# Kernel optimization log

Measured on AMD Instinct MI355X. Metric: run time of the kernel, lower is better.

## Reference

```python
import jax, jax.numpy as jnp
import numpy as np

B, T, C_EMBD, C_ATT = 16, 1024, 2048, 2048


def wkv(time_decay, time_first, k, v):
    """Numerically-stable RWKV WKV recurrence (matches wkv_cuda).
    time_decay/time_first: [C]; k, v: [B, T, C] -> y: [B, T, C]."""
    w = -jnp.exp(time_decay)  # [C], decay is -exp(param)
    u = time_first
    Bn, Tn, Cn = k.shape

    def step(carry, kv_t):
        aa, bb, pp = carry          # each [B, C]
        kt, vt = kv_t               # [B, C]
        ww = u + kt
        p = jnp.maximum(pp, ww)
        e1 = jnp.exp(pp - p)
        e2 = jnp.exp(ww - p)
        y = (e1 * aa + e2 * vt) / (e1 * bb + e2)
        ww2 = pp + w
        p2 = jnp.maximum(ww2, kt)
        e1b = jnp.exp(ww2 - p2)
        e2b = jnp.exp(kt - p2)
        new = (e1b * aa + e2b * vt, e1b * bb + e2b, p2)
        return new, y

    init = (jnp.zeros((Bn, Cn), k.dtype),
            jnp.zeros((Bn, Cn), k.dtype),
            jnp.full((Bn, Cn), -1e38, k.dtype))
    kT = jnp.swapaxes(k, 0, 1)  # [T, B, C]
    vT = jnp.swapaxes(v, 0, 1)
    _, ys = jax.lax.scan(step, init, (kT, vT))
    return jnp.swapaxes(ys, 0, 1)  # [B, T, C]


def setup_inputs() -> dict:
    key = jax.random.key(0)
    ks = jax.random.split(key, 10)
    xav = np.sqrt(2.0 / (C_EMBD + C_ATT))
    inp = {
        "x": jax.random.normal(ks[0], (B, T, C_EMBD), jnp.float32),
        "time_decay": jax.random.normal(ks[1], (C_ATT,), jnp.float32) * 0.02,
        "time_first": jax.random.normal(ks[2], (C_ATT,), jnp.float32) * 0.02,
        "time_mix_k": jax.random.normal(ks[3], (1, 1, C_EMBD), jnp.float32) * 0.02,
        "time_mix_v": jax.random.normal(ks[4], (1, 1, C_EMBD), jnp.float32) * 0.02,
        "time_mix_r": jax.random.normal(ks[5], (1, 1, C_EMBD), jnp.float32) * 0.02,
        "key_w": jax.random.normal(ks[6], (C_ATT, C_EMBD), jnp.float32) * xav,
        "value_w": jax.random.normal(ks[7], (C_ATT, C_EMBD), jnp.float32) * xav,
        "receptance_w": jax.random.normal(ks[8], (C_ATT, C_EMBD), jnp.float32) * xav,
        "output_w": jax.random.normal(ks[9], (C_EMBD, C_ATT), jnp.float32) * xav,
    }
    return inp


def reference(x, time_decay, time_first, time_mix_k, time_mix_v, time_mix_r,
              key_w, value_w, receptance_w, output_w):
    # time shift: xx[:, t] = x[:, t-1], xx[:, 0] = 0
    xx = jnp.pad(x, ((0, 0), (1, 0), (0, 0)))[:, :-1]
    xk = x * time_mix_k + xx * (1 - time_mix_k)
    xv = x * time_mix_v + xx * (1 - time_mix_v)
    xr = x * time_mix_r + xx * (1 - time_mix_r)
    k = jnp.einsum('btc,dc->btd', xk, key_w)
    v = jnp.einsum('btc,dc->btd', xv, value_w)
    r = jnp.einsum('btc,dc->btd', xr, receptance_w)
    sr = jax.nn.sigmoid(r)
    rwkv = sr * wkv(time_decay, time_first, k, v)
    return jnp.einsum('btd,cd->btc', rwkv, output_w)
```

## Files before the change

kernel.cpp:

```cpp
#include <hip/hip_runtime.h>
#include <hip/hip_bf16.h>

#define BB 16
#define TT 1024
#define CC 2048
#define TS 32

typedef __attribute__((ext_vector_type(4))) float f32x4;
typedef __attribute__((ext_vector_type(8))) short bf16x8;

__device__ __forceinline__ unsigned short f2bf(float f) {
  union { float f; unsigned u; } x; x.f = f;
  unsigned r = x.u + 0x7fffu + ((x.u >> 16) & 1u);
  return (unsigned short)(r >> 16);
}
__device__ __forceinline__ float bf2f(unsigned short u) {
  union { unsigned u; float f; } x; x.u = ((unsigned)u) << 16;
  return x.f;
}

__device__ __forceinline__ ushort4 mix4(float4 a, float4 b, float4 m) {
  ushort4 o;
  o.x = f2bf(a.x * m.x + b.x * (1.f - m.x));
  o.y = f2bf(a.y * m.y + b.y * (1.f - m.y));
  o.z = f2bf(a.z * m.z + b.z * (1.f - m.z));
  o.w = f2bf(a.w * m.w + b.w * (1.f - m.w));
  return o;
}

__global__ void f2bf_all(const float* __restrict__ w0, const float* __restrict__ w1,
                         const float* __restrict__ w2, const float* __restrict__ w3,
                         unsigned short* __restrict__ o0, unsigned short* __restrict__ o1,
                         unsigned short* __restrict__ o2, unsigned short* __restrict__ o3,
                         int n4each) {
  const float* ws[4] = {w0, w1, w2, w3};
  unsigned short* os[4] = {o0, o1, o2, o3};
  int total = 4 * n4each;
  for (int i = blockIdx.x * blockDim.x + threadIdx.x; i < total;
       i += gridDim.x * blockDim.x) {
    int seg = i / n4each, j = i - seg * n4each;
    float4 v = ((const float4*)ws[seg])[j];
    ushort4 o;
    o.x = f2bf(v.x); o.y = f2bf(v.y); o.z = f2bf(v.z); o.w = f2bf(v.w);
    ((ushort4*)os[seg])[j] = o;
  }
}

__global__ void mix_kernel(const float* __restrict__ x,
                           const float* __restrict__ tmk,
                           const float* __restrict__ tmv,
                           const float* __restrict__ tmr,
                           unsigned short* __restrict__ xk,
                           unsigned short* __restrict__ xv,
                           unsigned short* __restrict__ xr,
                           int t0, int Tc) {
  const int C4 = CC / 4;
  const int total = BB * Tc * C4;
  for (int g = blockIdx.x * blockDim.x + threadIdx.x; g < total;
       g += gridDim.x * blockDim.x) {
    int cg = g % C4;
    int lrow = g / C4;
    int tl = lrow % Tc;
    int b = lrow / Tc;
    int t = t0 + tl;
    size_t gidx = (size_t)(b * TT + t) * C4 + cg;
    float4 xc = ((const float4*)x)[gidx];
    float4 xp = make_float4(0.f, 0.f, 0.f, 0.f);
    if (t > 0) xp = ((const float4*)x)[gidx - C4];
    ((ushort4*)xk)[g] = mix4(xc, xp, ((const float4*)tmk)[cg]);
    ((ushort4*)xv)[g] = mix4(xc, xp, ((const float4*)tmv)[cg]);
    ((ushort4*)xr)[g] = mix4(xc, xp, ((const float4*)tmr)[cg]);
  }
}

template<bool BF16OUT>
__global__ __launch_bounds__(512, 2)
void gemm256(const unsigned short* __restrict__ A,
             const unsigned short* __restrict__ B,
             void* __restrict__ Cv, int M, int N, int K,
             int tcShift, int t0) {
  __shared__ __align__(1024) unsigned char lds[131072];
  const int tid = threadIdx.x;
  const int lane = tid & 63;
  const int wid = tid >> 6;
  const int wr = wid >> 2;
  const int wc = wid & 3;

  const int nwg = gridDim.x;
  const int cpx = nwg >> 3;
  const int bid = blockIdx.x;
  const int wg = (bid & 7) * cpx + (bid >> 3);
  const int bcolN = N >> 8;
  const int brow = wg / bcolN;
  const int bcol = wg % bcolN;

  const unsigned short* Ag = A + (size_t)(brow * 256) * K;
  const unsigned short* Bg = B + (size_t)(bcol * 256) * K;

  const int srow = tid >> 3;
  const int scolB = ((tid & 7) * 16) ^ ((srow & 7) << 4);
  const int scolE = scolB >> 1;
  const int ldsWave = wid * 1024;

#define STAGE(gbase, rowOff, ldsOff, kOff)                                     \
  __builtin_amdgcn_global_load_lds(                                            \
      (const __attribute__((address_space(1))) void*)(                         \
          (gbase) + (size_t)((rowOff) + srow) * K + (kOff) + scolE),           \
      (__attribute__((address_space(3))) void*)(lds + (ldsOff) + ldsWave),     \
      16, 0, 0)

  const int frow = lane & 15;
  const int fhi = (lane >> 4) << 4;

#define FRAG(tb, row, kk)                                                      \
  (*(const bf16x8*)(lds + (tb) + (row) * 128 +                                 \
                    ((((kk) << 6) + fhi) ^ (((row) & 7) << 4))))

  const int NT = K >> 6;

  STAGE(Bg,   0, 32768 +     0, 0);
  STAGE(Bg,  64, 32768 +  8192, 0);
  STAGE(Bg, 128, 32768 + 16384, 0);
  STAGE(Bg, 192, 32768 + 24576, 0);
  STAGE(Ag,   0,             0, 0);
  STAGE(Ag, 128,         16384, 0);
  STAGE(Ag,  64,          8192, 0);
  STAGE(Ag, 192,         24576, 0);

  f32x4 acc[8][4] = {};
  bf16x8 af[8], bfr[8];

  for (int kt = 0; kt < NT; ++kt) {
    const int p = kt & 1;
    const int Ab = p * 65536;
    const int Bb = Ab + 32768;
    const int An = (p ^ 1) * 65536;
    const int Bn = An + 32768;
    const int kN = (kt + 1) << 6;
    const bool st = (kt + 1 < NT);

    asm volatile("s_waitcnt vmcnt(2)" ::: "memory");
    __builtin_amdgcn_s_barrier();

    if (st) { STAGE(Bg, 0, Bn, kN); STAGE(Bg, 64, Bn + 8192, kN); }
#pragma unroll
    for (int m = 0; m < 4; ++m)
#pragma unroll
      for (int kk = 0; kk < 2; ++kk)
        af[m * 2 + kk] = FRAG(Ab, wr * 128 + m * 16 + frow, kk);
#pragma unroll
    for (int n = 0; n < 2; ++n)
#pragma unroll
      for (int kk = 0; kk < 2; ++kk)
        bfr[n * 2 + kk] = FRAG(Bb, wc * 64 + n * 16 + frow, kk);
    __builtin_amdgcn_s_setprio(1);
#pragma unroll
    for (int m = 0; m < 4; ++m)
#pragma unroll
      for (int n = 0; n < 2; ++n)
#pragma unroll
        for (int kk = 0; kk < 2; ++kk)
          acc[m][n] = __builtin_amdgcn_mfma_f32_16x16x32_bf16(
              af[m * 2 + kk], bfr[n * 2 + kk], acc[m][n], 0, 0, 0);
    __builtin_amdgcn_s_setprio(0);
    __builtin_amdgcn_s_barrier();

    if (st) { STAGE(Bg, 128, Bn + 16384, kN); STAGE(Bg, 192, Bn + 24576, kN); }
#pragma unroll
    for (int n = 2; n < 4; ++n)
#pragma unroll
      for (int kk = 0; kk < 2; ++kk)
        bfr[n * 2 + kk] = FRAG(Bb, wc * 64 + n * 16 + frow, kk);
    __builtin_amdgcn_s_setprio(1);
#pragma unroll
    for (int m = 0; m < 4; ++m)
#pragma unroll
      for (int n = 2; n < 4; ++n)
#pragma unroll
        for (int kk = 0; kk < 2; ++kk)
          acc[m][n] = __builtin_amdgcn_mfma_f32_16x16x32_bf16(
              af[m * 2 + kk], bfr[n * 2 + kk], acc[m][n], 0, 0, 0);
    __builtin_amdgcn_s_setprio(0);

    if (st) { asm volatile("s_waitcnt vmcnt(4)" ::: "memory"); }
    else    { asm volatile("s_waitcnt vmcnt(0)" ::: "memory"); }
    __builtin_amdgcn_s_barrier();

    if (st) { STAGE(Ag, 0, An, kN); STAGE(Ag, 128, An + 16384, kN); }
#pragma unroll
    for (int m = 0; m < 4; ++m)
#pragma unroll
      for (int kk = 0; kk < 2; ++kk)
        af[m * 2 + kk] = FRAG(Ab, wr * 128 + 64 + m * 16 + frow, kk);
    __builtin_amdgcn_s_setprio(1);
#pragma unroll
    for (int m = 0; m < 4; ++m)
#pragma unroll
      for (int n = 2; n < 4; ++n)
#pragma unroll
        for (int kk = 0; kk < 2; ++kk)
          acc[4 + m][n] = __builtin_amdgcn_mfma_f32_16x16x32_bf16(
              af[m * 2 + kk], bfr[n * 2 + kk], acc[4 + m][n], 0, 0, 0);
    __builtin_amdgcn_s_setprio(0);
    __builtin_amdgcn_s_barrier();

    if (st) { STAGE(Ag, 64, An + 8192, kN); STAGE(Ag, 192, An + 24576, kN); }
    __builtin_amdgcn_s_setprio(1);
#pragma unroll
    for (int m = 0; m < 4; ++m)
#pragma unroll
      for (int n = 0; n < 2; ++n)
#pragma unroll
        for (int kk = 0; kk < 2; ++kk)
          acc[4 + m][n] = __builtin_amdgcn_mfma_f32_16x16x32_bf16(
              af[m * 2 + kk], bfr[n * 2 + kk], acc[4 + m][n], 0, 0, 0);
    __builtin_amdgcn_s_setprio(0);
  }
#undef STAGE
#undef FRAG

  const int crow0 = (lane >> 4) << 2;
  const int ccol = lane & 15;
  const int tcMask = (1 << tcShift) - 1;
#pragma unroll
  for (int m = 0; m < 8; ++m)
#pragma unroll
    for (int n = 0; n < 4; ++n) {
      const int col = bcol * 256 + wc * 64 + n * 16 + ccol;
#pragma unroll
      for (int j = 0; j < 4; ++j) {
        int r = brow * 256 + wr * 128 + m * 16 + crow0 + j;
        int orow = ((r >> tcShift) << 10) + t0 + (r & tcMask);
        if (BF16OUT)
          ((unsigned short*)Cv)[(size_t)orow * N + col] = f2bf(acc[m][n][j]);
        else
          ((float*)Cv)[(size_t)orow * N + col] = acc[m][n][j];
      }
    }
}

__global__ void wkv_part(const float* __restrict__ time_decay,
                         const float* __restrict__ k,
                         const unsigned short* __restrict__ v,
                         float* __restrict__ paA, float* __restrict__ paB,
                         float* __restrict__ paP, int Tc) {
  int idx = blockIdx.x * blockDim.x + threadIdx.x;
  int c = idx & (CC - 1);
  int b = (idx >> 11) & (BB - 1);
  int s = idx >> 15;
  float w = -__expf(time_decay[c]);
  float aa = 0.f, bb = 0.f, pp = -1e38f;
  size_t base = ((size_t)b * Tc + s * TS) * CC + c;
  for (int t = 0; t < TS; ++t) {
    size_t off = base + (size_t)t * CC;
    float kt = k[off], vt = bf2f(v[off]);
    float ww2 = pp + w;
    float p2 = fmaxf(ww2, kt);
    float e1 = __expf(ww2 - p2), e2 = __expf(kt - p2);
    aa = e1 * aa + e2 * vt;
    bb = e1 * bb + e2;
    pp = p2;
  }
  paA[idx] = aa; paB[idx] = bb; paP[idx] = pp;
}

__global__ void wkv_comb(const float* __restrict__ time_decay,
                         const float* __restrict__ paA,
                         const float* __restrict__ paB,
                         const float* __restrict__ paP,
                         float* __restrict__ inA, float* __restrict__ inB,
                         float* __restrict__ inP,
                         float* __restrict__ state, int S, int t0) {
  int idx = blockIdx.x * blockDim.x + threadIdx.x;
  int c = idx & (CC - 1);
  float w = -__expf(time_decay[c]);
  float wTs = w * (float)TS;
  float A, Bv, P;
  if (t0 == 0) { A = 0.f; Bv = 0.f; P = -1e38f; }
  else { A = state[idx]; Bv = state[32768 + idx]; P = state[65536 + idx]; }
  for (int s = 0; s < S; ++s) {
    size_t o = (size_t)s * 32768 + idx;
    inA[o] = A; inB[o] = Bv; inP[o] = P;
    float Pd = P + wTs;
    float Ps = paP[o];
    float Pn = fmaxf(Pd, Ps);
    float e1 = __expf(Pd - Pn), e2 = __expf(Ps - Pn);
    A = e1 * A + e2 * paA[o];
    Bv = e1 * Bv + e2 * paB[o];
    P = Pn;
  }
  state[idx] = A; state[32768 + idx] = Bv; state[65536 + idx] = P;
}

__global__ void wkv_out(const float* __restrict__ time_decay,
                        const float* __restrict__ time_first,
                        const float* __restrict__ k,
                        const unsigned short* __restrict__ v,
                        const unsigned short* __restrict__ r,
                        unsigned short* __restrict__ rwkv,
                        const float* __restrict__ inA,
                        const float* __restrict__ inB,
                        const float* __restrict__ inP, int Tc) {
  int idx = blockIdx.x * blockDim.x + threadIdx.x;
  int c = idx & (CC - 1);
  int b = (idx >> 11) & (BB - 1);
  int s = idx >> 15;
  float w = -__expf(time_decay[c]);
  float u = time_first[c];
  float aa = inA[idx], bb = inB[idx], pp = inP[idx];
  size_t base = ((size_t)b * Tc + s * TS) * CC + c;
  for (int t = 0; t < TS; ++t) {
    size_t off = base + (size_t)t * CC;
    float kt = k[off], vt = bf2f(v[off]);
    float ww = u + kt;
    float p = fmaxf(pp, ww);
    float e1 = __expf(pp - p), e2 = __expf(ww - p);
    float y = (e1 * aa + e2 * vt) / (e1 * bb + e2);
    float rr = bf2f(r[off]);
    float sr = 1.f / (1.f + __expf(-rr));
    rwkv[off] = f2bf(sr * y);
    float ww2 = pp + w;
    float p2 = fmaxf(ww2, kt);
    float e1b = __expf(ww2 - p2), e2b = __expf(kt - p2);
    aa = e1b * aa + e2b * vt;
    bb = e1b * bb + e2b;
    pp = p2;
  }
}

extern "C" void kernel_launch(void* const* d_in, const int* in_sizes, int n_in,
                              void* d_out, int out_size, void* d_ws,
                              size_t ws_size, hipStream_t stream) {
  const float* x          = (const float*)d_in[0];
  const float* time_decay = (const float*)d_in[1];
  const float* time_first = (const float*)d_in[2];
  const float* tmk        = (const float*)d_in[3];
  const float* tmv        = (const float*)d_in[4];
  const float* tmr        = (const float*)d_in[5];
  const float* key_w      = (const float*)d_in[6];
  const float* value_w    = (const float*)d_in[7];
  const float* rec_w      = (const float*)d_in[8];
  const float* out_w      = (const float*)d_in[9];
  float* out = (float*)d_out;

  const size_t WW = (size_t)CC * CC;
  const size_t wtBytes = 4 * WW * 2;
  const size_t stBytes = 3 * (size_t)BB * CC * 4;

  int Tc = 1024;
  while (Tc > 32) {
    size_t chunkBytes = (size_t)BB * Tc * CC * 14;
    if (wtBytes + stBytes + chunkBytes + 1024 <= ws_size) break;
    Tc >>= 1;
  }
  const int Mc = BB * Tc;
  const size_t NC = (size_t)Mc * CC;
  const int S = Tc / TS;

  char* p = (char*)d_ws;
  unsigned short* wk  = (unsigned short*)p; p += WW * 2;
  unsigned short* wv  = (unsigned short*)p; p += WW * 2;
  unsigned short* wrr = (unsigned short*)p; p += WW * 2;
  unsigned short* wo  = (unsigned short*)p; p += WW * 2;
  float* state        = (float*)p;          p += stBytes;
  float* kbuf         = (float*)p;          p += NC * 4;
  unsigned short* vbuf= (unsigned short*)p; p += NC * 2;
  unsigned short* xk  = (unsigned short*)p; p += NC * 2;
  unsigned short* xv  = (unsigned short*)p; p += NC * 2;
  unsigned short* xr  = (unsigned short*)p; p += NC * 2;
  unsigned short* rbuf= (unsigned short*)p; p += NC * 2;
  unsigned short* rwkv = xk;

  const size_t SBt = (size_t)S * 32768;
  float* paA = (float*)xv;
  float* paB = paA + SBt;
  float* paP = paB + SBt;
  float* inA = paP + SBt;
  float* inB = inA + SBt;
  float* inP = inB + SBt;

  f2bf_all<<<2048, 256, 0, stream>>>(key_w, value_w, rec_w, out_w,
                                     wk, wv, wrr, wo, (int)(WW / 4));

  int tcShift = 0;
  while ((1 << tcShift) < Tc) ++tcShift;

  const int nwg = (Mc / 256) * (CC / 256);
  int mixBlocks = (Mc * (CC / 4) + 255) / 256;
  if (mixBlocks > 4096) mixBlocks = 4096;

  for (int t0 = 0; t0 < TT; t0 += Tc) {
    mix_kernel<<<mixBlocks, 256, 0, stream>>>(x, tmk, tmv, tmr, xk, xv, xr,
                                              t0, Tc);
    gemm256<false><<<nwg, 512, 0, stream>>>(xk, wk, kbuf, Mc, CC, CC, 10, 0);
    gemm256<true><<<nwg, 512, 0, stream>>>(xv, wv, vbuf, Mc, CC, CC, 10, 0);
    wkv_part<<<S * 128, 256, 0, stream>>>(time_decay, kbuf, vbuf,
                                          paA, paB, paP, Tc);
    gemm256<true><<<nwg, 512, 0, stream>>>(xr, wrr, rbuf, Mc, CC, CC, 10, 0);
    wkv_comb<<<128, 256, 0, stream>>>(time_decay, paA, paB, paP,
                                      inA, inB, inP, state, S, t0);
    wkv_out<<<S * 128, 256, 0, stream>>>(time_decay, time_first, kbuf, vbuf,
                                         rbuf, rwkv, inA, inB, inP, Tc);
    gemm256<false><<<nwg, 512, 0, stream>>>(rwkv, wo, out, Mc, CC, CC,
                                            tcShift, t0);
  }
}
```

Before: 740.1 us.

## Software-pipeline GEMM fragment loads across iterations and store k in bf16

Restructures the GEMM main loop so the first A/B fragments for the next k-tile are read from LDS at the end of the current iteration. The output quadrant order is reordered so fragment reads overlap MFMA work, with barriers and waitcnts moved to match. Separately, the key projection output is now written as bf16 instead of fp32, shrinking kbuf traffic and workspace size. This risks precision loss in the exponent-sensitive WKV recurrence and adds register pressure from the double fragment sets.

```diff
diff --git a/kernel.cpp b/kernel.cpp
--- a/kernel.cpp
+++ b/kernel.cpp
@@ -116,6 +116,8 @@
   (*(const bf16x8*)(lds + (tb) + (row) * 128 +                                 \
                     ((((kk) << 6) + fhi) ^ (((row) & 7) << 4))))
 
+#define FENCE asm volatile("" ::: "memory")
+
   const int NT = K >> 6;
 
   STAGE(Bg,   0, 32768 +     0, 0);
@@ -128,119 +130,134 @@
   STAGE(Ag, 192,         24576, 0);
 
   f32x4 acc[8][4] = {};
-  bf16x8 af[8], bfr[8];
+  bf16x8 af0[8], af1[8], bf0[4], bf1[4];
+
+  asm volatile("s_waitcnt vmcnt(2)" ::: "memory");
+  __builtin_amdgcn_s_barrier();
+#pragma unroll
+  for (int m = 0; m < 4; ++m)
+#pragma unroll
+    for (int kk = 0; kk < 2; ++kk)
+      af0[m * 2 + kk] = FRAG(0, wr * 128 + m * 16 + frow, kk);
+#pragma unroll
+  for (int n = 0; n < 2; ++n)
+#pragma unroll
+    for (int kk = 0; kk < 2; ++kk)
+      bf0[n * 2 + kk] = FRAG(32768, wc * 64 + n * 16 + frow, kk);
 
   for (int kt = 0; kt < NT; ++kt) {
-    const int p = kt & 1;
-    const int Ab = p * 65536;
-    const int Bb = Ab + 32768;
-    const int An = (p ^ 1) * 65536;
-    const int Bn = An + 32768;
+    const int cur = (kt & 1) << 16;
+    const int nxt = ((kt + 1) & 1) << 16;
     const int kN = (kt + 1) << 6;
     const bool st = (kt + 1 < NT);
 
-    asm volatile("s_waitcnt vmcnt(2)" ::: "memory");
-    __builtin_amdgcn_s_barrier();
-
-    if (st) { STAGE(Bg, 0, Bn, kN); STAGE(Bg, 64, Bn + 8192, kN); }
+    if (st) { STAGE(Bg, 0, nxt + 32768, kN); STAGE(Bg, 64, nxt + 32768 + 8192, kN); }
+    __builtin_amdgcn_s_setprio(1);
 #pragma unroll
     for (int m = 0; m < 4; ++m)
 #pragma unroll
+      for (int n = 0; n < 2; ++n)
+#pragma unroll
+        for (int kk = 0; kk < 2; ++kk)
+          acc[m][n] = __builtin_amdgcn_mfma_f32_16x16x32_bf16(
+              af0[m * 2 + kk], bf0[n * 2 + kk], acc[m][n], 0, 0, 0);
+    __builtin_amdgcn_s_setprio(0);
+#pragma unroll
+    for (int n = 0; n < 2; ++n)
+#pragma unroll
       for (int kk = 0; kk < 2; ++kk)
-        af[m * 2 + kk] = FRAG(Ab, wr * 128 + m * 16 + frow, kk);
-#pragma unroll
-    for (int n = 0; n < 2; ++n)
-#pragma unroll
-      for (int kk = 0; kk < 2; ++kk)
-        bfr[n * 2 + kk] = FRAG(Bb, wc * 64 + n * 16 + frow, kk);
-    __builtin_amdgcn_s_setprio(1);
-#pragma unroll
-    for (int m = 0; m < 4; ++m)
-#pragma unroll
-      for (int n = 0; n < 2; ++n)
-#pragma unroll
-        for (int kk = 0; kk < 2; ++kk)
-          acc[m][n] = __builtin_amdgcn_mfma_f32_16x16x32_bf16(
-              af[m * 2 + kk], bfr[n * 2 + kk], acc[m][n], 0, 0, 0);
-    __builtin_amdgcn_s_setprio(0);
-    __builtin_amdgcn_s_barrier();
-
-    if (st) { STAGE(Bg, 128, Bn + 16384, kN); STAGE(Bg, 192, Bn + 24576, kN); }
-#pragma unroll
-    for (int n = 2; n < 4; ++n)
-#pragma unroll
-      for (int kk = 0; kk < 2; ++kk)
-        bfr[n * 2 + kk] = FRAG(Bb, wc * 64 + n * 16 + frow, kk);
-    __builtin_amdgcn_s_setprio(1);
-#pragma unroll
-    for (int m = 0; m < 4; ++m)
-#pragma unroll
-      for (int n = 2; n < 4; ++n)
-#pragma unroll
-        for (int kk = 0; kk < 2; ++kk)
-          acc[m][n] = __builtin_amdgcn_mfma_f32_16x16x32_bf16(
-              af[m * 2 + kk], bfr[n * 2 + kk], acc[m][n], 0, 0, 0);
-    __builtin_amdgcn_s_setprio(0);
-
-    if (st) { asm volatile("s_waitcnt vmcnt(4)" ::: "memory"); }
+        bf1[n * 2 + kk] = FRAG(cur + 32768, wc * 64 + 32 + n * 16 + frow, kk);
+    FENCE;
+    if (st) { asm volatile("s_waitcnt vmcnt(2)" ::: "memory"); }
     else    { asm volatile("s_waitcnt vmcnt(0)" ::: "memory"); }
     __builtin_amdgcn_s_barrier();
 
-    if (st) { STAGE(Ag, 0, An, kN); STAGE(Ag, 128, An + 16384, kN); }
+    if (st) { STAGE(Bg, 128, nxt + 32768 + 16384, kN); STAGE(Bg, 192, nxt + 32768 + 24576, kN); }
 #pragma unroll
     for (int m = 0; m < 4; ++m)
 #pragma unroll
       for (int kk = 0; kk < 2; ++kk)
-        af[m * 2 + kk] = FRAG(Ab, wr * 128 + 64 + m * 16 + frow, kk);
+        af1[m * 2 + kk] = FRAG(cur, wr * 128 + 64 + m * 16 + frow, kk);
     __builtin_amdgcn_s_setprio(1);
 #pragma unroll
     for (int m = 0; m < 4; ++m)
 #pragma unroll
-      for (int n = 2; n < 4; ++n)
+      for (int n = 0; n < 2; ++n)
+#pragma unroll
+        for (int kk = 0; kk < 2; ++kk)
+          acc[m][2 + n] = __builtin_amdgcn_mfma_f32_16x16x32_bf16(
+              af0[m * 2 + kk], bf1[n * 2 + kk], acc[m][2 + n], 0, 0, 0);
+    __builtin_amdgcn_s_setprio(0);
+    FENCE;
+    __builtin_amdgcn_s_barrier();
+
+    if (st) { STAGE(Ag, 0, nxt, kN); STAGE(Ag, 128, nxt + 16384, kN); }
+    __builtin_amdgcn_s_setprio(1);
+#pragma unroll
+    for (int m = 0; m < 4; ++m)
+#pragma unroll
+      for (int n = 0; n < 2; ++n)
+#pragma unroll
+        for (int kk = 0; kk < 2; ++kk)
+          acc[4 + m][2 + n] = __builtin_amdgcn_mfma_f32_16x16x32_bf16(
+              af1[m * 2 + kk], bf1[n * 2 + kk], acc[4 + m][2 + n], 0, 0, 0);
+    __builtin_amdgcn_s_setprio(0);
+    FENCE;
+    __builtin_amdgcn_s_barrier();
+
+    if (st) { STAGE(Ag, 64, nxt + 8192, kN); STAGE(Ag, 192, nxt + 24576, kN); }
+    __builtin_amdgcn_s_setprio(1);
+#pragma unroll
+    for (int m = 0; m < 4; ++m)
+#pragma unroll
+      for (int n = 0; n < 2; ++n)
 #pragma unroll
         for (int kk = 0; kk < 2; ++kk)
           acc[4 + m][n] = __builtin_amdgcn_mfma_f32_16x16x32_bf16(
-              af[m * 2 + kk], bfr[n * 2 + kk], acc[4 + m][n], 0, 0, 0);
+              af1[m * 2 + kk], bf0[n * 2 + kk], acc[4 + m][n], 0, 0, 0);
     __builtin_amdgcn_s_setprio(0);
-    __builtin_amdgcn_s_barrier();
-
-    if (st) { STAGE(Ag, 64, An + 8192, kN); STAGE(Ag, 192, An + 24576, kN); }
-    __builtin_amdgcn_s_setprio(1);
-#pragma unroll
-    for (int m = 0; m < 4; ++m)
+    if (st) {
+      asm volatile("s_waitcnt vmcnt(2)" ::: "memory");
+      __builtin_amdgcn_s_barrier();
+#pragma unroll
+      for (int m = 0; m < 4; ++m)
+#pragma unroll
+        for (int kk = 0; kk < 2; ++kk)
+          af0[m * 2 + kk] = FRAG(nxt, wr * 128 + m * 16 + frow, kk);
 #pragma unroll
       for (int n = 0; n < 2; ++n)
 #pragma unroll
         for (int kk = 0; kk < 2; ++kk)
-          acc[4 + m][n] = __builtin_amdgcn_mfma_f32_16x16x32_bf16(
-              af[m * 2 + kk], bfr[n * 2 + kk], acc[4 + m][n], 0, 0, 0);
-    __builtin_amdgcn_s_setprio(0);
+          bf0[n * 2 + kk] = FRAG(nxt + 32768, wc * 64 + n * 16 + frow, kk);
+      FENCE;
+    }
   }
 #undef STAGE
 #undef FRAG
+#undef FENCE
 
   const int crow0 = (lane >> 4) << 2;
   const int ccol = lane & 15;
   const int tcMask = (1 << tcShift) - 1;
 #pragma unroll
-  for (int m = 0; m < 8; ++m)
-#pragma unroll
-    for (int n = 0; n < 4; ++n) {
-      const int col = bcol * 256 + wc * 64 + n * 16 + ccol;
+  for (int am = 0; am < 8; ++am)
+#pragma unroll
+    for (int an = 0; an < 4; ++an) {
+      const int col = bcol * 256 + wc * 64 + (an >> 1) * 32 + (an & 1) * 16 + ccol;
 #pragma unroll
       for (int j = 0; j < 4; ++j) {
-        int r = brow * 256 + wr * 128 + m * 16 + crow0 + j;
+        int r = brow * 256 + wr * 128 + (am >> 2) * 64 + (am & 3) * 16 + crow0 + j;
         int orow = ((r >> tcShift) << 10) + t0 + (r & tcMask);
         if (BF16OUT)
-          ((unsigned short*)Cv)[(size_t)orow * N + col] = f2bf(acc[m][n][j]);
+          ((unsigned short*)Cv)[(size_t)orow * N + col] = f2bf(acc[am][an][j]);
         else
-          ((float*)Cv)[(size_t)orow * N + col] = acc[m][n][j];
+          ((float*)Cv)[(size_t)orow * N + col] = acc[am][an][j];
       }
     }
 }
 
 __global__ void wkv_part(const float* __restrict__ time_decay,
-                         const float* __restrict__ k,
+                         const unsigned short* __restrict__ k,
                          const unsigned short* __restrict__ v,
                          float* __restrict__ paA, float* __restrict__ paB,
                          float* __restrict__ paP, int Tc) {
@@ -253,7 +270,7 @@
   size_t base = ((size_t)b * Tc + s * TS) * CC + c;
   for (int t = 0; t < TS; ++t) {
     size_t off = base + (size_t)t * CC;
-    float kt = k[off], vt = bf2f(v[off]);
+    float kt = bf2f(k[off]), vt = bf2f(v[off]);
     float ww2 = pp + w;
     float p2 = fmaxf(ww2, kt);
     float e1 = __expf(ww2 - p2), e2 = __expf(kt - p2);
@@ -294,7 +311,7 @@
 
 __global__ void wkv_out(const float* __restrict__ time_decay,
                         const float* __restrict__ time_first,
-                        const float* __restrict__ k,
+                        const unsigned short* __restrict__ k,
                         const unsigned short* __restrict__ v,
                         const unsigned short* __restrict__ r,
                         unsigned short* __restrict__ rwkv,
@@ -311,7 +328,7 @@
   size_t base = ((size_t)b * Tc + s * TS) * CC + c;
   for (int t = 0; t < TS; ++t) {
     size_t off = base + (size_t)t * CC;
-    float kt = k[off], vt = bf2f(v[off]);
+    float kt = bf2f(k[off]), vt = bf2f(v[off]);
     float ww = u + kt;
     float p = fmaxf(pp, ww);
     float e1 = __expf(pp - p), e2 = __expf(ww - p);
@@ -349,7 +366,7 @@
 
   int Tc = 1024;
   while (Tc > 32) {
-    size_t chunkBytes = (size_t)BB * Tc * CC * 14;
+    size_t chunkBytes = (size_t)BB * Tc * CC * 12;
     if (wtBytes + stBytes + chunkBytes + 1024 <= ws_size) break;
     Tc >>= 1;
   }
@@ -363,7 +380,7 @@
   unsigned short* wrr = (unsigned short*)p; p += WW * 2;
   unsigned short* wo  = (unsigned short*)p; p += WW * 2;
   float* state        = (float*)p;          p += stBytes;
-  float* kbuf         = (float*)p;          p += NC * 4;
+  unsigned short* kbuf= (unsigned short*)p; p += NC * 2;
   unsigned short* vbuf= (unsigned short*)p; p += NC * 2;
   unsigned short* xk  = (unsigned short*)p; p += NC * 2;
   unsigned short* xv  = (unsigned short*)p; p += NC * 2;
@@ -392,7 +409,7 @@
   for (int t0 = 0; t0 < TT; t0 += Tc) {
     mix_kernel<<<mixBlocks, 256, 0, stream>>>(x, tmk, tmv, tmr, xk, xv, xr,
                                               t0, Tc);
-    gemm256<false><<<nwg, 512, 0, stream>>>(xk, wk, kbuf, Mc, CC, CC, 10, 0);
+    gemm256<true><<<nwg, 512, 0, stream>>>(xk, wk, kbuf, Mc, CC, CC, 10, 0);
     gemm256<true><<<nwg, 512, 0, stream>>>(xv, wv, vbuf, Mc, CC, CC, 10, 0);
     wkv_part<<<S * 128, 256, 0, stream>>>(time_decay, kbuf, vbuf,
                                           paA, paB, paP, Tc);
```

Result: no change. 728.1 us (-1.6%).
